# Optimization experiments

Hardware: AMD Instinct MI355X
Metric: run time of the kernel (lower is better)

The kernel has to match this reference:

```python
import math
import jax, jax.numpy as jnp
from jax import lax
import numpy as np

B = 2048
C = 32000
TAU = math.log(32000.0)
LAM = 1.0
BATCH_SIZE = 2048.0
TEMP = 4.0


def lambertw(y, iters=8):
    """Principal-branch Lambert W for real y >= -1/e via Halley iterations."""
    # branch-point expansion init for small y, asymptotic log init for large y
    ey1 = jnp.maximum(jnp.e * y + 1.0, 0.0)
    w_small = -1.0 + jnp.sqrt(2.0 * ey1)
    ys = jnp.maximum(y, 1.0 + 1e-6)
    w_big = jnp.log(ys) - jnp.log(jnp.maximum(jnp.log(ys), 1e-6))
    w = jnp.where(y < 1.0, w_small, w_big)
    for _ in range(iters):
        ew = jnp.exp(w)
        f = w * ew - y
        wp1 = w + 1.0
        denom = ew * wp1 - (w + 2.0) * f / (2.0 * jnp.where(jnp.abs(wp1) > 1e-6, wp1, 1e-6))
        denom = jnp.where(jnp.abs(denom) > 1e-12, denom, 1e-12)
        w = w - f / denom
    return w


def _per_sample_loss(logits, teacher_outputs, targets, ones):
    # cross entropy per sample
    logp = jax.nn.log_softmax(logits, axis=-1)  # [B, C]
    ce = -jnp.take_along_axis(logp, targets[:, None], axis=1)[:, 0]  # [B]
    # temperature-scaled KL(teacher || student), summed over classes
    logp_T = jax.nn.log_softmax(logits / TEMP, axis=-1)
    p_t = jax.nn.softmax(teacher_outputs / TEMP, axis=-1)
    kl = jnp.sum(p_t * (jnp.log(p_t) - logp_T), axis=-1)  # [B]
    return ones[:, 0] * ce + TEMP * TEMP * ones[:, 1] * kl  # [B]


def reference(logits, teacher_outputs, targets, ones):
    base = _per_sample_loss(logits, teacher_outputs, targets, ones)  # [B]
    # sigma computed from detached loss (torch .detach() + cpu numpy round-trip)
    l_i = lax.stop_gradient(base)
    y = 0.5 * jnp.maximum(-2.0 / jnp.e, (l_i - TAU) / LAM)
    sigma = jnp.exp(-lambertw(y))  # [B], no gradient flows through
    loss = (base - TAU) * sigma + LAM * jnp.log(sigma) ** 2
    return loss.sum() / BATCH_SIZE


def setup_inputs() -> dict:
    key = jax.random.key(0)
    k1, k2, k3 = jax.random.split(key, 3)
    return {
        "logits": jax.random.normal(k1, (B, C), dtype=jnp.float32),
        "teacher_outputs": jax.random.normal(k2, (B, C), dtype=jnp.float32),
        "targets": jax.random.randint(k3, (B,), 0, C, dtype=jnp.int32),
        "ones": jnp.ones((B, 2), dtype=jnp.float32),
    }
```

## Files before the change

kernel.cpp:

```cpp
#include <hip/hip_runtime.h>
#include <math.h>

#define NCLASS 32000
#define NROWS  2048
#define T1     320
#define U      5
#define STAGES 5

#define TAU_D 10.373491181781864
#define E_D   2.718281828459045

__device__ __forceinline__ double lambertw_d(double y) {
    double ey1 = fmax(E_D * y + 1.0, 0.0);
    double w_small = -1.0 + sqrt(2.0 * ey1);
    double ys = fmax(y, 1.0 + 1e-6);
    double ly = log(ys);
    double w_big = ly - log(fmax(ly, 1e-6));
    double w = (y < 1.0) ? w_small : w_big;
#pragma unroll
    for (int i = 0; i < 8; ++i) {
        double ew = exp(w);
        double f = w * ew - y;
        double wp1 = w + 1.0;
        double safe_wp1 = (fabs(wp1) > 1e-6) ? wp1 : 1e-6;
        double denom = ew * wp1 - (w + 2.0) * f / (2.0 * safe_wp1);
        if (!(fabs(denom) > 1e-12)) denom = 1e-12;
        w = w - f / denom;
    }
    return w;
}

__device__ __forceinline__ void upd(float x, float t,
                                    float& s1, float& sT, float& st,
                                    float& A, float& Bv) {
    float ex4 = __expf(x * 0.25f);
    float ex2 = ex4 * ex4;
    s1 += ex2 * ex2;
    sT += ex4;
    float et = __expf(t * 0.25f);
    st += et;
    A  = fmaf(et, t, A);
    Bv = fmaf(et, x, Bv);
}

__global__ __launch_bounds__(T1) void sums_kernel(
    const float* __restrict__ logits,
    const float* __restrict__ teacher,
    float* __restrict__ ws)
{
    const int row = blockIdx.x;
    const size_t base = (size_t)row * NCLASS;
    const float4* __restrict__ lg = (const float4*)(logits  + base);
    const float4* __restrict__ tc = (const float4*)(teacher + base);
    const int tid = threadIdx.x;

    float s1 = 0.f, sT = 0.f, st = 0.f, A = 0.f, Bv = 0.f;
    float4 xa[U], ta[U], xb[U], tb[U];

    auto load_stage = [&](float4* xd, float4* td, int s) {
#pragma unroll
        for (int k = 0; k < U; ++k) {
            const int j = tid + (s * U + k) * T1;
            xd[k] = lg[j];
            td[k] = tc[j];
        }
    };
    auto compute_stage = [&](const float4* xd, const float4* td) {
#pragma unroll
        for (int k = 0; k < U; ++k) {
            upd(xd[k].x, td[k].x, s1, sT, st, A, Bv);
            upd(xd[k].y, td[k].y, s1, sT, st, A, Bv);
            upd(xd[k].z, td[k].z, s1, sT, st, A, Bv);
            upd(xd[k].w, td[k].w, s1, sT, st, A, Bv);
        }
    };

    load_stage(xa, ta, 0);
    load_stage(xb, tb, 1);
    compute_stage(xa, ta);
    load_stage(xa, ta, 2);
    compute_stage(xb, tb);
    load_stage(xb, tb, 3);
    compute_stage(xa, ta);
    load_stage(xa, ta, 4);
    compute_stage(xb, tb);
    compute_stage(xa, ta);

#pragma unroll
    for (int off = 32; off > 0; off >>= 1) {
        s1 += __shfl_down(s1, off);
        sT += __shfl_down(sT, off);
        st += __shfl_down(st, off);
        A  += __shfl_down(A,  off);
        Bv += __shfl_down(Bv, off);
    }

    __shared__ float red[T1 / 64][5];
    const int wave = tid >> 6;
    const int lane = tid & 63;
    if (lane == 0) {
        red[wave][0] = s1; red[wave][1] = sT; red[wave][2] = st;
        red[wave][3] = A;  red[wave][4] = Bv;
    }
    __syncthreads();

    if (tid < 5) {
        float acc = 0.f;
#pragma unroll
        for (int w = 0; w < T1 / 64; ++w) acc += red[w][tid];
        ws[row * 5 + tid] = acc;
    }
}

__global__ __launch_bounds__(256) void finalize_kernel(
    const float* __restrict__ logits,
    const int*   __restrict__ targets,
    const float* __restrict__ ones,
    const float* __restrict__ ws,
    float* __restrict__ out)
{
    const int r = blockIdx.x * 256 + threadIdx.x;

    const float fs1 = ws[r * 5 + 0];
    const float fsT = ws[r * 5 + 1];
    const float fst = ws[r * 5 + 2];
    const float fA  = ws[r * 5 + 3];
    const float fB  = ws[r * 5 + 4];

    const float xt = logits[(size_t)r * NCLASS + (size_t)targets[r]];
    const float o0 = ones[2 * r + 0];
    const float o1 = ones[2 * r + 1];

    const double lse   = log((double)fs1);
    const double lseT  = log((double)fsT);
    const double lseTt = log((double)fst);

    const double ce = lse - (double)xt;
    const double kl = ((double)fA - (double)fB) / ((double)fst * 4.0)
                      - lseTt + lseT;

    const double base = (double)o0 * ce + 16.0 * (double)o1 * kl;

    const double y = 0.5 * fmax(-2.0 / E_D, (base - TAU_D));
    const double w = lambertw_d(y);
    const double sigma = exp(-w);
    double loss = (base - TAU_D) * sigma + w * w;

#pragma unroll
    for (int off = 32; off > 0; off >>= 1)
        loss += __shfl_down(loss, off);

    __shared__ double red2[4];
    const int wave = threadIdx.x >> 6;
    const int lane = threadIdx.x & 63;
    if (lane == 0) red2[wave] = loss;
    __syncthreads();

    if (threadIdx.x == 0) {
        double acc = red2[0] + red2[1] + red2[2] + red2[3];
        atomicAdd(out, (float)(acc / 2048.0));
    }
}

extern "C" void kernel_launch(void* const* d_in, const int* in_sizes, int n_in,
                              void* d_out, int out_size, void* d_ws, size_t ws_size,
                              hipStream_t stream) {
    const float* logits  = (const float*)d_in[0];
    const float* teacher = (const float*)d_in[1];
    const int*   targets = (const int*)d_in[2];
    const float* ones    = (const float*)d_in[3];
    float* out = (float*)d_out;
    float* ws  = (float*)d_ws;

    hipMemsetAsync(out, 0, sizeof(float) * (size_t)out_size, stream);

    sums_kernel<<<NROWS, T1, 0, stream>>>(logits, teacher, ws);
    finalize_kernel<<<NROWS / 256, 256, 0, stream>>>(logits, targets, ones, ws, out);
}
```

Measured before the change: 502.3 us.

## Split each row across four blocks and issue all loads up front

The per-row reduction is split into four segments, each handled by its own 256-thread block, giving four times as many blocks. Each thread loads all of its eight float4 pairs before computing instead of using the staged double-buffer schedule. The finalize kernel sums the four partial results per row. This raises parallelism and the number of loads in flight, at the cost of more workspace traffic, some idle lanes in the last tile of each segment, and higher register use.

```diff
diff --git a/kernel.cpp b/kernel.cpp
--- a/kernel.cpp
+++ b/kernel.cpp
@@ -3,9 +3,10 @@
 
 #define NCLASS 32000
 #define NROWS  2048
-#define T1     320
-#define U      5
-#define STAGES 5
+#define NSEG   4
+#define SEGF4  2000
+#define T1     256
+#define KPT    8
 
 #define TAU_D 10.373491181781864
 #define E_D   2.718281828459045
@@ -48,43 +49,32 @@
     const float* __restrict__ teacher,
     float* __restrict__ ws)
 {
-    const int row = blockIdx.x;
+    const int row = blockIdx.x >> 2;
+    const int seg = blockIdx.x & 3;
     const size_t base = (size_t)row * NCLASS;
-    const float4* __restrict__ lg = (const float4*)(logits  + base);
-    const float4* __restrict__ tc = (const float4*)(teacher + base);
+    const float4* __restrict__ lg = (const float4*)(logits  + base) + seg * SEGF4;
+    const float4* __restrict__ tc = (const float4*)(teacher + base) + seg * SEGF4;
     const int tid = threadIdx.x;
 
+    float4 xv[KPT], tv[KPT];
+#pragma unroll
+    for (int k = 0; k < KPT; ++k) {
+        int j = tid + k * T1;
+        int jc = j < SEGF4 ? j : (SEGF4 - 1);
+        xv[k] = lg[jc];
+        tv[k] = tc[jc];
+    }
+
     float s1 = 0.f, sT = 0.f, st = 0.f, A = 0.f, Bv = 0.f;
-    float4 xa[U], ta[U], xb[U], tb[U];
-
-    auto load_stage = [&](float4* xd, float4* td, int s) {
 #pragma unroll
-        for (int k = 0; k < U; ++k) {
-            const int j = tid + (s * U + k) * T1;
-            xd[k] = lg[j];
-            td[k] = tc[j];
+    for (int k = 0; k < KPT; ++k) {
+        if (tid + k * T1 < SEGF4) {
+            upd(xv[k].x, tv[k].x, s1, sT, st, A, Bv);
+            upd(xv[k].y, tv[k].y, s1, sT, st, A, Bv);
+            upd(xv[k].z, tv[k].z, s1, sT, st, A, Bv);
+            upd(xv[k].w, tv[k].w, s1, sT, st, A, Bv);
         }
-    };
-    auto compute_stage = [&](const float4* xd, const float4* td) {
-#pragma unroll
-        for (int k = 0; k < U; ++k) {
-            upd(xd[k].x, td[k].x, s1, sT, st, A, Bv);
-            upd(xd[k].y, td[k].y, s1, sT, st, A, Bv);
-            upd(xd[k].z, td[k].z, s1, sT, st, A, Bv);
-            upd(xd[k].w, td[k].w, s1, sT, st, A, Bv);
-        }
-    };
-
-    load_stage(xa, ta, 0);
-    load_stage(xb, tb, 1);
-    compute_stage(xa, ta);
-    load_stage(xa, ta, 2);
-    compute_stage(xb, tb);
-    load_stage(xb, tb, 3);
-    compute_stage(xa, ta);
-    load_stage(xa, ta, 4);
-    compute_stage(xb, tb);
-    compute_stage(xa, ta);
+    }
 
 #pragma unroll
     for (int off = 32; off > 0; off >>= 1) {
@@ -108,7 +98,7 @@
         float acc = 0.f;
 #pragma unroll
         for (int w = 0; w < T1 / 64; ++w) acc += red[w][tid];
-        ws[row * 5 + tid] = acc;
+        ws[(size_t)blockIdx.x * 5 + tid] = acc;
     }
 }
 
@@ -121,11 +111,12 @@
 {
     const int r = blockIdx.x * 256 + threadIdx.x;
 
-    const float fs1 = ws[r * 5 + 0];
-    const float fsT = ws[r * 5 + 1];
-    const float fst = ws[r * 5 + 2];
-    const float fA  = ws[r * 5 + 3];
-    const float fB  = ws[r * 5 + 4];
+    float fs1 = 0.f, fsT = 0.f, fst = 0.f, fA = 0.f, fB = 0.f;
+#pragma unroll
+    for (int s = 0; s < NSEG; ++s) {
+        const float* p = ws + ((size_t)r * NSEG + s) * 5;
+        fs1 += p[0]; fsT += p[1]; fst += p[2]; fA += p[3]; fB += p[4];
+    }
 
     const float xt = logits[(size_t)r * NCLASS + (size_t)targets[r]];
     const float o0 = ones[2 * r + 0];
@@ -174,6 +165,6 @@
 
     hipMemsetAsync(out, 0, sizeof(float) * (size_t)out_size, stream);
 
-    sums_kernel<<<NROWS, T1, 0, stream>>>(logits, teacher, ws);
+    sums_kernel<<<NROWS * NSEG, T1, 0, stream>>>(logits, teacher, ws);
     finalize_kernel<<<NROWS / 256, 256, 0, stream>>>(logits, targets, ones, ws, out);
 }
```

New measurement: 503.6 us. No clear change (+0.3%).
